# Optimization experiments

Measured on AMD Instinct MI355X. Metric: run time of the kernel, lower is better.

## Reference

```python
import jax, jax.numpy as jnp
import numpy as np

N_NODES = 50000
N_EDGES = 800000
NODE_DIM = 128
EDGE_DIM = 64
HIDDEN = 256


def setup_inputs() -> dict:
    key = jax.random.key(0)
    ks = jax.random.split(key, 12)
    glorot = lambda k, fi, fo: jax.random.normal(k, (fi, fo), jnp.float32) * (2.0 / (fi + fo)) ** 0.5
    return {
        "node_features": jax.random.normal(ks[0], (N_NODES, NODE_DIM), jnp.float32),
        "edge_features": jax.random.normal(ks[1], (N_EDGES, EDGE_DIM), jnp.float32),
        "src": jax.random.randint(ks[2], (N_EDGES,), 0, N_NODES),
        "dst": jax.random.randint(ks[3], (N_EDGES,), 0, N_NODES),
        # edge_update MLP: (2*node_dim + edge_dim) -> hidden -> edge_dim
        "We1": glorot(ks[4], 2 * NODE_DIM + EDGE_DIM, HIDDEN),
        "be1": jnp.zeros((HIDDEN,), jnp.float32),
        "We2": glorot(ks[5], HIDDEN, EDGE_DIM),
        "be2": jnp.zeros((EDGE_DIM,), jnp.float32),
        # node_update MLP: (node_dim + edge_dim) -> hidden -> node_dim
        "Wn1": glorot(ks[6], NODE_DIM + EDGE_DIM, HIDDEN),
        "bn1": jnp.zeros((HIDDEN,), jnp.float32),
        "Wn2": glorot(ks[7], HIDDEN, NODE_DIM),
        "bn2": jnp.zeros((NODE_DIM,), jnp.float32),
    }


def reference(node_features, edge_features, src, dst, We1, be1, We2, be2, Wn1, bn1, Wn2, bn2):
    # message: per-edge MLP on [src_h, e, dst_h]
    concat = jnp.concatenate(
        [node_features[src], edge_features, node_features[dst]], axis=1
    )  # [E, 2*node_dim + edge_dim]
    e_upd = jax.nn.relu(concat @ We1 + be1) @ We2 + be2  # [E, edge_dim]

    # reduce: sum incoming messages per destination node
    e_sum = jax.ops.segment_sum(e_upd, dst, num_segments=node_features.shape[0])  # [N, edge_dim]
    node_in = jnp.concatenate([node_features, e_sum], axis=1)  # [N, node_dim + edge_dim]
    h_new = jax.nn.relu(node_in @ Wn1 + bn1) @ Wn2 + bn2  # [N, node_dim]

    # DGL only applies reduce_func to nodes with at least one incoming edge
    deg = jax.ops.segment_sum(jnp.ones_like(dst, jnp.float32), dst, num_segments=node_features.shape[0])
    h_out = jnp.where(deg[:, None] > 0, h_new, node_features)

    # original module never writes e_updated back: returned edge features are the inputs
    return h_out, edge_features
```

## Files before the change

kernel.cpp:

```cpp
#include <hip/hip_runtime.h>

#define N_NODES 50000
#define N_EDGES 800000
#define NODE_DIM 128
#define EDGE_DIM 64
#define HIDDEN 256
#define K_E 320
#define K_N 192

typedef __attribute__((ext_vector_type(8))) short bf16x8;
typedef __attribute__((ext_vector_type(4))) float f32x4;
typedef unsigned short u16;
typedef unsigned int u32;

__device__ inline u16 f2bf(float f) {
  u32 u = __builtin_bit_cast(u32, f);
  u += 0x7fffu + ((u >> 16) & 1u);
  return (u16)(u >> 16);
}

__device__ inline void st_bf4(u16* p, float4 v) {
  ushort4 r;
  r.x = f2bf(v.x); r.y = f2bf(v.y); r.z = f2bf(v.z); r.w = f2bf(v.w);
  *reinterpret_cast<ushort4*>(p) = r;
}

__global__ void prep_weights(const float* __restrict__ We1, const float* __restrict__ We2,
                             const float* __restrict__ Wn1, const float* __restrict__ Wn2,
                             u16* __restrict__ we1t, u16* __restrict__ we2t,
                             u16* __restrict__ wn1t, u16* __restrict__ wn2t) {
  const int stride = gridDim.x * blockDim.x;
  const int tid = blockIdx.x * blockDim.x + threadIdx.x;
  for (int i = tid; i < HIDDEN * K_E; i += stride) {
    int n = i / K_E, k = i % K_E;
    we1t[i] = f2bf(We1[k * HIDDEN + n]);
  }
  for (int i = tid; i < EDGE_DIM * HIDDEN; i += stride) {
    int n = i / HIDDEN, k = i % HIDDEN;
    we2t[i] = f2bf(We2[k * EDGE_DIM + n]);
  }
  for (int i = tid; i < HIDDEN * K_N; i += stride) {
    int n = i / K_N, k = i % K_N;
    wn1t[i] = f2bf(Wn1[k * HIDDEN + n]);
  }
  for (int i = tid; i < NODE_DIM * HIDDEN; i += stride) {
    int n = i / HIDDEN, k = i % HIDDEN;
    wn2t[i] = f2bf(Wn2[k * NODE_DIM + n]);
  }
}

#define SA_E 328
#define SH   264

__global__ __launch_bounds__(256) void edge_kernel(
    const float* __restrict__ nf, const float* __restrict__ ef,
    const int* __restrict__ src, const int* __restrict__ dst,
    const u16* __restrict__ w1, const float* __restrict__ b1,
    const u16* __restrict__ w2, const float* __restrict__ b2,
    float* __restrict__ e_sum, float* __restrict__ degf,
    float* __restrict__ out_edge)
{
  __shared__ u16 A[64 * SA_E];
  __shared__ int sidx[64], didx[64];
  const int tid = threadIdx.x;
  const int e0 = blockIdx.x * 64;

  if (tid < 64) { sidx[tid] = src[e0 + tid]; didx[tid] = dst[e0 + tid]; }
  __syncthreads();

  const float4* nf4 = reinterpret_cast<const float4*>(nf);
  const float4* ef4 = reinterpret_cast<const float4*>(ef);
  float4* oe4 = reinterpret_cast<float4*>(out_edge);

  {
    int row = tid >> 5, c4 = tid & 31;
    #pragma unroll
    for (int p = 0; p < 8; ++p, row += 8) {
      float4 v = nf4[(size_t)sidx[row] * 32 + c4];
      st_bf4(&A[row * SA_E + c4 * 4], v);
    }
  }
  {
    #pragma unroll
    for (int p = 0; p < 4; ++p) {
      int idx = p * 256 + tid;
      int row = idx >> 4, c4 = idx & 15;
      size_t g = (size_t)(e0 + row) * 16 + c4;
      float4 v = ef4[g];
      oe4[g] = v;
      st_bf4(&A[row * SA_E + 128 + c4 * 4], v);
    }
  }
  {
    int row = tid >> 5, c4 = tid & 31;
    #pragma unroll
    for (int p = 0; p < 8; ++p, row += 8) {
      float4 v = nf4[(size_t)didx[row] * 32 + c4];
      st_bf4(&A[row * SA_E + 192 + c4 * 4], v);
    }
  }
  if (tid < 64) degf[didx[tid]] = 1.0f;
  __syncthreads();

  const int wave = tid >> 6, lane = tid & 63;
  const int lr = lane & 15;
  const int lk = (lane >> 4) * 8;

  f32x4 acc[4][4] = {};
  for (int kb = 0; kb < K_E / 32; ++kb) {
    const int ko = kb * 32 + lk;
    bf16x8 a[4], b[4];
    #pragma unroll
    for (int mt = 0; mt < 4; ++mt)
      a[mt] = *reinterpret_cast<const bf16x8*>(&A[(mt * 16 + lr) * SA_E + ko]);
    #pragma unroll
    for (int nt = 0; nt < 4; ++nt)
      b[nt] = *reinterpret_cast<const bf16x8*>(&w1[(size_t)(wave * 64 + nt * 16 + lr) * K_E + ko]);
    #pragma unroll
    for (int mt = 0; mt < 4; ++mt)
      #pragma unroll
      for (int nt = 0; nt < 4; ++nt)
        acc[mt][nt] = __builtin_amdgcn_mfma_f32_16x16x32_bf16(a[mt], b[nt], acc[mt][nt], 0, 0, 0);
  }
  __syncthreads();

  u16* H = A;
  #pragma unroll
  for (int mt = 0; mt < 4; ++mt)
    #pragma unroll
    for (int nt = 0; nt < 4; ++nt) {
      int col = wave * 64 + nt * 16 + lr;
      float bias = b1[col];
      #pragma unroll
      for (int j = 0; j < 4; ++j) {
        int row = mt * 16 + (lane >> 4) * 4 + j;
        float h = acc[mt][nt][j] + bias;
        H[row * SH + col] = f2bf(h > 0.f ? h : 0.f);
      }
    }
  __syncthreads();

  f32x4 acc2[4] = {};
  for (int kb = 0; kb < HIDDEN / 32; ++kb) {
    const int ko = kb * 32 + lk;
    bf16x8 a = *reinterpret_cast<const bf16x8*>(&H[(wave * 16 + lr) * SH + ko]);
    #pragma unroll
    for (int nt = 0; nt < 4; ++nt) {
      bf16x8 b = *reinterpret_cast<const bf16x8*>(&w2[(size_t)(nt * 16 + lr) * HIDDEN + ko]);
      acc2[nt] = __builtin_amdgcn_mfma_f32_16x16x32_bf16(a, b, acc2[nt], 0, 0, 0);
    }
  }
  #pragma unroll
  for (int nt = 0; nt < 4; ++nt) {
    int col = nt * 16 + lr;
    float bias = b2[col];
    #pragma unroll
    for (int j = 0; j < 4; ++j) {
      int row = wave * 16 + (lane >> 4) * 4 + j;
      atomicAdd(&e_sum[(size_t)didx[row] * 64 + col], acc2[nt][j] + bias);
    }
  }
}

#define SA_N 200

__global__ __launch_bounds__(256) void node_kernel(
    const float* __restrict__ nf, const float* __restrict__ e_sum,
    const float* __restrict__ degf,
    const u16* __restrict__ w1, const float* __restrict__ b1,
    const u16* __restrict__ w2, const float* __restrict__ b2,
    float* __restrict__ hout)
{
  __shared__ u16 A[64 * SH];
  const int tid = threadIdx.x;
  const int n0 = blockIdx.x * 64;

  const float4* nf4 = reinterpret_cast<const float4*>(nf);
  const float4* es4 = reinterpret_cast<const float4*>(e_sum);

  {
    int row = tid >> 5, c4 = tid & 31;
    #pragma unroll
    for (int p = 0; p < 8; ++p, row += 8) {
      int rg = min(n0 + row, N_NODES - 1);
      float4 v = nf4[(size_t)rg * 32 + c4];
      st_bf4(&A[row * SA_N + c4 * 4], v);
    }
  }
  {
    #pragma unroll
    for (int p = 0; p < 4; ++p) {
      int idx = p * 256 + tid;
      int row = idx >> 4, c4 = idx & 15;
      int rg = min(n0 + row, N_NODES - 1);
      float4 v = es4[(size_t)rg * 16 + c4];
      st_bf4(&A[row * SA_N + 128 + c4 * 4], v);
    }
  }
  __syncthreads();

  const int wave = tid >> 6, lane = tid & 63;
  const int lr = lane & 15;
  const int lk = (lane >> 4) * 8;

  f32x4 acc[4][4] = {};
  for (int kb = 0; kb < K_N / 32; ++kb) {
    const int ko = kb * 32 + lk;
    bf16x8 a[4], b[4];
    #pragma unroll
    for (int mt = 0; mt < 4; ++mt)
      a[mt] = *reinterpret_cast<const bf16x8*>(&A[(mt * 16 + lr) * SA_N + ko]);
    #pragma unroll
    for (int nt = 0; nt < 4; ++nt)
      b[nt] = *reinterpret_cast<const bf16x8*>(&w1[(size_t)(wave * 64 + nt * 16 + lr) * K_N + ko]);
    #pragma unroll
    for (int mt = 0; mt < 4; ++mt)
      #pragma unroll
      for (int nt = 0; nt < 4; ++nt)
        acc[mt][nt] = __builtin_amdgcn_mfma_f32_16x16x32_bf16(a[mt], b[nt], acc[mt][nt], 0, 0, 0);
  }
  __syncthreads();

  u16* H = A;
  #pragma unroll
  for (int mt = 0; mt < 4; ++mt)
    #pragma unroll
    for (int nt = 0; nt < 4; ++nt) {
      int col = wave * 64 + nt * 16 + lr;
      float bias = b1[col];
      #pragma unroll
      for (int j = 0; j < 4; ++j) {
        int row = mt * 16 + (lane >> 4) * 4 + j;
        float h = acc[mt][nt][j] + bias;
        H[row * SH + col] = f2bf(h > 0.f ? h : 0.f);
      }
    }
  __syncthreads();

  f32x4 acc2[8] = {};
  for (int kb = 0; kb < HIDDEN / 32; ++kb) {
    const int ko = kb * 32 + lk;
    bf16x8 a = *reinterpret_cast<const bf16x8*>(&H[(wave * 16 + lr) * SH + ko]);
    #pragma unroll
    for (int nt = 0; nt < 8; ++nt) {
      bf16x8 b = *reinterpret_cast<const bf16x8*>(&w2[(size_t)(nt * 16 + lr) * HIDDEN + ko]);
      acc2[nt] = __builtin_amdgcn_mfma_f32_16x16x32_bf16(a, b, acc2[nt], 0, 0, 0);
    }
  }
  #pragma unroll
  for (int nt = 0; nt < 8; ++nt) {
    int col = nt * 16 + lr;
    float bias = b2[col];
    #pragma unroll
    for (int j = 0; j < 4; ++j) {
      int row = wave * 16 + (lane >> 4) * 4 + j;
      int rg = n0 + row;
      if (rg < N_NODES) {
        float v = acc2[nt][j] + bias;
        hout[(size_t)rg * NODE_DIM + col] =
            (degf[rg] > 0.f) ? v : nf[(size_t)rg * NODE_DIM + col];
      }
    }
  }
}

extern "C" void kernel_launch(void* const* d_in, const int* in_sizes, int n_in,
                              void* d_out, int out_size, void* d_ws, size_t ws_size,
                              hipStream_t stream) {
  const float* nf  = (const float*)d_in[0];
  const float* ef  = (const float*)d_in[1];
  const int*   src = (const int*)d_in[2];
  const int*   dst = (const int*)d_in[3];
  const float* We1 = (const float*)d_in[4];
  const float* be1 = (const float*)d_in[5];
  const float* We2 = (const float*)d_in[6];
  const float* be2 = (const float*)d_in[7];
  const float* Wn1 = (const float*)d_in[8];
  const float* bn1 = (const float*)d_in[9];
  const float* Wn2 = (const float*)d_in[10];
  const float* bn2 = (const float*)d_in[11];

  char* ws = (char*)d_ws;
  float* e_sum = (float*)ws;
  float* degf  = (float*)(ws + 12800000);
  u16*  we1t   = (u16*)(ws + 13000000);
  u16*  we2t   = (u16*)(ws + 13163840);
  u16*  wn1t   = (u16*)(ws + 13196608);
  u16*  wn2t   = (u16*)(ws + 13294912);

  float* hout = (float*)d_out;
  float* out_edge = hout + (size_t)N_NODES * NODE_DIM;

  hipMemsetAsync(ws, 0, 13000000, stream);
  prep_weights<<<128, 256, 0, stream>>>(We1, We2, Wn1, Wn2, we1t, we2t, wn1t, wn2t);
  edge_kernel<<<N_EDGES / 64, 256, 0, stream>>>(nf, ef, src, dst, we1t, be1, we2t, be2,
                                                e_sum, degf, out_edge);
  node_kernel<<<(N_NODES + 63) / 64, 256, 0, stream>>>(nf, e_sum, degf, wn1t, bn1,
                                                       wn2t, bn2, hout);
}
```

Baseline: 631.3 us.

## Replace atomic segment-sum with counting-sort CSR gather and widen edge blocks

Builds a CSR layout of edges by destination (histogram, single-block scan, atomic rank scatter). The edge kernel then writes bf16 messages into their sorted slots, and the node kernel sums each node's messages by walking its segment, instead of issuing float atomics into e_sum. The edge kernel also moves to 512 threads with a new wave tiling (8 waves, each covering 16 rows by 128 columns). The sorted path only runs when the workspace is large enough, otherwise the atomic path is kept. It adds extra small kernels, a serial single-block scan, and bf16 rounding of each message before summation.

```diff
diff --git a/kernel.cpp b/kernel.cpp
--- a/kernel.cpp
+++ b/kernel.cpp
@@ -18,7 +18,10 @@
   u += 0x7fffu + ((u >> 16) & 1u);
   return (u16)(u >> 16);
 }
-
+__device__ inline float bf2f(u16 u) {
+  u32 x = ((u32)u) << 16;
+  return __builtin_bit_cast(float, x);
+}
 __device__ inline void st_bf4(u16* p, float4 v) {
   ushort4 r;
   r.x = f2bf(v.x); r.y = f2bf(v.y); r.z = f2bf(v.z); r.w = f2bf(v.w);
@@ -49,73 +52,252 @@
   }
 }
 
+__global__ void hist_kernel(const int* __restrict__ dst, int* __restrict__ hist) {
+  int e = blockIdx.x * blockDim.x + threadIdx.x;
+  if (e < N_EDGES) atomicAdd(&hist[dst[e]], 1);
+}
+
+#define SCAN_T 256
+#define SCAN_ITEMS 196
+__global__ void scan_kernel(const int* __restrict__ hist, int* __restrict__ off,
+                            int* __restrict__ cursor) {
+  __shared__ int ssum[SCAN_T];
+  const int tid = threadIdx.x;
+  const int base = tid * SCAN_ITEMS;
+  int s = 0;
+  for (int i = 0; i < SCAN_ITEMS; ++i) {
+    int idx = base + i;
+    s += (idx < N_NODES) ? hist[idx] : 0;
+  }
+  ssum[tid] = s;
+  __syncthreads();
+  for (int d = 1; d < SCAN_T; d <<= 1) {
+    int t = (tid >= d) ? ssum[tid - d] : 0;
+    __syncthreads();
+    ssum[tid] += t;
+    __syncthreads();
+  }
+  int run = ssum[tid] - s;
+  for (int i = 0; i < SCAN_ITEMS; ++i) {
+    int idx = base + i;
+    if (idx < N_NODES) {
+      off[idx] = run;
+      cursor[idx] = run;
+      run += hist[idx];
+    }
+  }
+  if (tid == SCAN_T - 1) off[N_NODES] = run;
+}
+
+__global__ void scatter_kernel(const int* __restrict__ dst, int* __restrict__ cursor,
+                               int* __restrict__ rank) {
+  int e = blockIdx.x * blockDim.x + threadIdx.x;
+  if (e < N_EDGES) rank[e] = atomicAdd(&cursor[dst[e]], 1);
+}
+
 #define SA_E 328
 #define SH   264
 
-__global__ __launch_bounds__(256) void edge_kernel(
+__global__ __launch_bounds__(512, 5) void edge_kernel(
     const float* __restrict__ nf, const float* __restrict__ ef,
     const int* __restrict__ src, const int* __restrict__ dst,
     const u16* __restrict__ w1, const float* __restrict__ b1,
     const u16* __restrict__ w2, const float* __restrict__ b2,
+    const int* __restrict__ rank, u16* __restrict__ e_upd,
     float* __restrict__ e_sum, float* __restrict__ degf,
-    float* __restrict__ out_edge)
+    int sorted, float* __restrict__ out_edge)
 {
   __shared__ u16 A[64 * SA_E];
-  __shared__ int sidx[64], didx[64];
+  __shared__ u16 H2[64 * 68];
+  __shared__ int sidx[64], didx[64], rk[64];
   const int tid = threadIdx.x;
   const int e0 = blockIdx.x * 64;
 
-  if (tid < 64) { sidx[tid] = src[e0 + tid]; didx[tid] = dst[e0 + tid]; }
+  if (tid < 64) {
+    sidx[tid] = src[e0 + tid];
+    didx[tid] = dst[e0 + tid];
+    rk[tid] = sorted ? rank[e0 + tid] : 0;
+  }
   __syncthreads();
 
   const float4* nf4 = reinterpret_cast<const float4*>(nf);
   const float4* ef4 = reinterpret_cast<const float4*>(ef);
   float4* oe4 = reinterpret_cast<float4*>(out_edge);
 
-  {
-    int row = tid >> 5, c4 = tid & 31;
-    #pragma unroll
-    for (int p = 0; p < 8; ++p, row += 8) {
-      float4 v = nf4[(size_t)sidx[row] * 32 + c4];
-      st_bf4(&A[row * SA_E + c4 * 4], v);
-    }
-  }
-  {
-    #pragma unroll
-    for (int p = 0; p < 4; ++p) {
-      int idx = p * 256 + tid;
-      int row = idx >> 4, c4 = idx & 15;
-      size_t g = (size_t)(e0 + row) * 16 + c4;
-      float4 v = ef4[g];
-      oe4[g] = v;
-      st_bf4(&A[row * SA_E + 128 + c4 * 4], v);
-    }
-  }
-  {
-    int row = tid >> 5, c4 = tid & 31;
-    #pragma unroll
-    for (int p = 0; p < 8; ++p, row += 8) {
-      float4 v = nf4[(size_t)didx[row] * 32 + c4];
-      st_bf4(&A[row * SA_E + 192 + c4 * 4], v);
-    }
-  }
-  if (tid < 64) degf[didx[tid]] = 1.0f;
+  #pragma unroll
+  for (int p = 0; p < 4; ++p) {
+    int i = p * 512 + tid;
+    int row = i >> 5, c4 = i & 31;
+    float4 v = nf4[(size_t)sidx[row] * 32 + c4];
+    st_bf4(&A[row * SA_E + c4 * 4], v);
+  }
+  #pragma unroll
+  for (int p = 0; p < 2; ++p) {
+    int i = p * 512 + tid;
+    int row = i >> 4, c4 = i & 15;
+    size_t g = (size_t)(e0 + row) * 16 + c4;
+    float4 v = ef4[g];
+    oe4[g] = v;
+    st_bf4(&A[row * SA_E + 128 + c4 * 4], v);
+  }
+  #pragma unroll
+  for (int p = 0; p < 4; ++p) {
+    int i = p * 512 + tid;
+    int row = i >> 5, c4 = i & 31;
+    float4 v = nf4[(size_t)didx[row] * 32 + c4];
+    st_bf4(&A[row * SA_E + 192 + c4 * 4], v);
+  }
+  if (!sorted && tid < 64) degf[didx[tid]] = 1.0f;
   __syncthreads();
 
   const int wave = tid >> 6, lane = tid & 63;
   const int lr = lane & 15;
   const int lk = (lane >> 4) * 8;
 
-  f32x4 acc[4][4] = {};
+  const int wr = wave >> 1;
+  const int wc = wave & 1;
+  f32x4 acc[8] = {};
   for (int kb = 0; kb < K_E / 32; ++kb) {
     const int ko = kb * 32 + lk;
+    bf16x8 a = *reinterpret_cast<const bf16x8*>(&A[(wr * 16 + lr) * SA_E + ko]);
+    #pragma unroll
+    for (int nt = 0; nt < 8; ++nt) {
+      bf16x8 b = *reinterpret_cast<const bf16x8*>(
+          &w1[(size_t)(wc * 128 + nt * 16 + lr) * K_E + ko]);
+      acc[nt] = __builtin_amdgcn_mfma_f32_16x16x32_bf16(a, b, acc[nt], 0, 0, 0);
+    }
+  }
+  __syncthreads();
+
+  u16* H = A;
+  #pragma unroll
+  for (int nt = 0; nt < 8; ++nt) {
+    int col = wc * 128 + nt * 16 + lr;
+    float bias = b1[col];
+    #pragma unroll
+    for (int j = 0; j < 4; ++j) {
+      int row = wr * 16 + (lane >> 4) * 4 + j;
+      float h = acc[nt][j] + bias;
+      H[row * SH + col] = f2bf(h > 0.f ? h : 0.f);
+    }
+  }
+  __syncthreads();
+
+  const int r2 = wave >> 1;
+  const int c2 = wave & 1;
+  f32x4 acc2[2] = {};
+  for (int kb = 0; kb < HIDDEN / 32; ++kb) {
+    const int ko = kb * 32 + lk;
+    bf16x8 a = *reinterpret_cast<const bf16x8*>(&H[(r2 * 16 + lr) * SH + ko]);
+    #pragma unroll
+    for (int nt = 0; nt < 2; ++nt) {
+      bf16x8 b = *reinterpret_cast<const bf16x8*>(
+          &w2[(size_t)(c2 * 32 + nt * 16 + lr) * HIDDEN + ko]);
+      acc2[nt] = __builtin_amdgcn_mfma_f32_16x16x32_bf16(a, b, acc2[nt], 0, 0, 0);
+    }
+  }
+
+  if (sorted) {
+    #pragma unroll
+    for (int nt = 0; nt < 2; ++nt) {
+      int col = c2 * 32 + nt * 16 + lr;
+      float bias = b2[col];
+      #pragma unroll
+      for (int j = 0; j < 4; ++j) {
+        int row = r2 * 16 + (lane >> 4) * 4 + j;
+        H2[row * 68 + col] = f2bf(acc2[nt][j] + bias);
+      }
+    }
+    __syncthreads();
+    #pragma unroll
+    for (int p = 0; p < 2; ++p) {
+      int i = p * 512 + tid;
+      int row = i >> 4, c = (i & 15) * 4;
+      ushort4 v = *reinterpret_cast<ushort4*>(&H2[row * 68 + c]);
+      *reinterpret_cast<ushort4*>(&e_upd[(size_t)rk[row] * 64 + c]) = v;
+    }
+  } else {
+    #pragma unroll
+    for (int nt = 0; nt < 2; ++nt) {
+      int col = c2 * 32 + nt * 16 + lr;
+      float bias = b2[col];
+      #pragma unroll
+      for (int j = 0; j < 4; ++j) {
+        int row = r2 * 16 + (lane >> 4) * 4 + j;
+        atomicAdd(&e_sum[(size_t)didx[row] * 64 + col], acc2[nt][j] + bias);
+      }
+    }
+  }
+}
+
+#define SA_N 200
+
+__global__ __launch_bounds__(256) void node_kernel(
+    const float* __restrict__ nf,
+    const u16* __restrict__ e_upd, const int* __restrict__ off,
+    const int* __restrict__ hist,
+    const float* __restrict__ e_sum, const float* __restrict__ degf,
+    const u16* __restrict__ w1, const float* __restrict__ b1,
+    const u16* __restrict__ w2, const float* __restrict__ b2,
+    int sorted, float* __restrict__ hout)
+{
+  __shared__ u16 A[64 * SH];
+  const int tid = threadIdx.x;
+  const int n0 = blockIdx.x * 64;
+
+  const float4* nf4 = reinterpret_cast<const float4*>(nf);
+
+  #pragma unroll
+  for (int p = 0; p < 8; ++p) {
+    int i = p * 256 + tid;
+    int row = i >> 5, c4 = i & 31;
+    int rg = min(n0 + row, N_NODES - 1);
+    float4 v = nf4[(size_t)rg * 32 + c4];
+    st_bf4(&A[row * SA_N + c4 * 4], v);
+  }
+
+  if (sorted) {
+    const int g = tid >> 4, l16 = tid & 15;
+    for (int row = g; row < 64; row += 16) {
+      int n = n0 + row;
+      float4 acc = {0.f, 0.f, 0.f, 0.f};
+      if (n < N_NODES) {
+        int s0 = off[n], s1 = off[n + 1];
+        for (int s = s0; s < s1; ++s) {
+          ushort4 v = *reinterpret_cast<const ushort4*>(&e_upd[(size_t)s * 64 + l16 * 4]);
+          acc.x += bf2f(v.x); acc.y += bf2f(v.y);
+          acc.z += bf2f(v.z); acc.w += bf2f(v.w);
+        }
+      }
+      st_bf4(&A[row * SA_N + 128 + l16 * 4], acc);
+    }
+  } else {
+    const float4* es4 = reinterpret_cast<const float4*>(e_sum);
+    #pragma unroll
+    for (int p = 0; p < 4; ++p) {
+      int i = p * 256 + tid;
+      int row = i >> 4, c4 = i & 15;
+      int rg = min(n0 + row, N_NODES - 1);
+      float4 v = es4[(size_t)rg * 16 + c4];
+      st_bf4(&A[row * SA_N + 128 + c4 * 4], v);
+    }
+  }
+  __syncthreads();
+
+  const int wave = tid >> 6, lane = tid & 63;
+  const int lr = lane & 15;
+  const int lk = (lane >> 4) * 8;
+
+  f32x4 acc[4][4] = {};
+  for (int kb = 0; kb < K_N / 32; ++kb) {
+    const int ko = kb * 32 + lk;
     bf16x8 a[4], b[4];
     #pragma unroll
     for (int mt = 0; mt < 4; ++mt)
-      a[mt] = *reinterpret_cast<const bf16x8*>(&A[(mt * 16 + lr) * SA_E + ko]);
+      a[mt] = *reinterpret_cast<const bf16x8*>(&A[(mt * 16 + lr) * SA_N + ko]);
     #pragma unroll
     for (int nt = 0; nt < 4; ++nt)
-      b[nt] = *reinterpret_cast<const bf16x8*>(&w1[(size_t)(wave * 64 + nt * 16 + lr) * K_E + ko]);
+      b[nt] = *reinterpret_cast<const bf16x8*>(&w1[(size_t)(wave * 64 + nt * 16 + lr) * K_N + ko]);
     #pragma unroll
     for (int mt = 0; mt < 4; ++mt)
       #pragma unroll
@@ -140,103 +322,6 @@
     }
   __syncthreads();
 
-  f32x4 acc2[4] = {};
-  for (int kb = 0; kb < HIDDEN / 32; ++kb) {
-    const int ko = kb * 32 + lk;
-    bf16x8 a = *reinterpret_cast<const bf16x8*>(&H[(wave * 16 + lr) * SH + ko]);
-    #pragma unroll
-    for (int nt = 0; nt < 4; ++nt) {
-      bf16x8 b = *reinterpret_cast<const bf16x8*>(&w2[(size_t)(nt * 16 + lr) * HIDDEN + ko]);
-      acc2[nt] = __builtin_amdgcn_mfma_f32_16x16x32_bf16(a, b, acc2[nt], 0, 0, 0);
-    }
-  }
-  #pragma unroll
-  for (int nt = 0; nt < 4; ++nt) {
-    int col = nt * 16 + lr;
-    float bias = b2[col];
-    #pragma unroll
-    for (int j = 0; j < 4; ++j) {
-      int row = wave * 16 + (lane >> 4) * 4 + j;
-      atomicAdd(&e_sum[(size_t)didx[row] * 64 + col], acc2[nt][j] + bias);
-    }
-  }
-}
-
-#define SA_N 200
-
-__global__ __launch_bounds__(256) void node_kernel(
-    const float* __restrict__ nf, const float* __restrict__ e_sum,
-    const float* __restrict__ degf,
-    const u16* __restrict__ w1, const float* __restrict__ b1,
-    const u16* __restrict__ w2, const float* __restrict__ b2,
-    float* __restrict__ hout)
-{
-  __shared__ u16 A[64 * SH];
-  const int tid = threadIdx.x;
-  const int n0 = blockIdx.x * 64;
-
-  const float4* nf4 = reinterpret_cast<const float4*>(nf);
-  const float4* es4 = reinterpret_cast<const float4*>(e_sum);
-
-  {
-    int row = tid >> 5, c4 = tid & 31;
-    #pragma unroll
-    for (int p = 0; p < 8; ++p, row += 8) {
-      int rg = min(n0 + row, N_NODES - 1);
-      float4 v = nf4[(size_t)rg * 32 + c4];
-      st_bf4(&A[row * SA_N + c4 * 4], v);
-    }
-  }
-  {
-    #pragma unroll
-    for (int p = 0; p < 4; ++p) {
-      int idx = p * 256 + tid;
-      int row = idx >> 4, c4 = idx & 15;
-      int rg = min(n0 + row, N_NODES - 1);
-      float4 v = es4[(size_t)rg * 16 + c4];
-      st_bf4(&A[row * SA_N + 128 + c4 * 4], v);
-    }
-  }
-  __syncthreads();
-
-  const int wave = tid >> 6, lane = tid & 63;
-  const int lr = lane & 15;
-  const int lk = (lane >> 4) * 8;
-
-  f32x4 acc[4][4] = {};
-  for (int kb = 0; kb < K_N / 32; ++kb) {
-    const int ko = kb * 32 + lk;
-    bf16x8 a[4], b[4];
-    #pragma unroll
-    for (int mt = 0; mt < 4; ++mt)
-      a[mt] = *reinterpret_cast<const bf16x8*>(&A[(mt * 16 + lr) * SA_N + ko]);
-    #pragma unroll
-    for (int nt = 0; nt < 4; ++nt)
-      b[nt] = *reinterpret_cast<const bf16x8*>(&w1[(size_t)(wave * 64 + nt * 16 + lr) * K_N + ko]);
-    #pragma unroll
-    for (int mt = 0; mt < 4; ++mt)
-      #pragma unroll
-      for (int nt = 0; nt < 4; ++nt)
-        acc[mt][nt] = __builtin_amdgcn_mfma_f32_16x16x32_bf16(a[mt], b[nt], acc[mt][nt], 0, 0, 0);
-  }
-  __syncthreads();
-
-  u16* H = A;
-  #pragma unroll
-  for (int mt = 0; mt < 4; ++mt)
-    #pragma unroll
-    for (int nt = 0; nt < 4; ++nt) {
-      int col = wave * 64 + nt * 16 + lr;
-      float bias = b1[col];
-      #pragma unroll
-      for (int j = 0; j < 4; ++j) {
-        int row = mt * 16 + (lane >> 4) * 4 + j;
-        float h = acc[mt][nt][j] + bias;
-        H[row * SH + col] = f2bf(h > 0.f ? h : 0.f);
-      }
-    }
-  __syncthreads();
-
   f32x4 acc2[8] = {};
   for (int kb = 0; kb < HIDDEN / 32; ++kb) {
     const int ko = kb * 32 + lk;
@@ -256,9 +341,10 @@
       int row = wave * 16 + (lane >> 4) * 4 + j;
       int rg = n0 + row;
       if (rg < N_NODES) {
+        bool has_in = sorted ? (hist[rg] != 0) : (degf[rg] > 0.f);
         float v = acc2[nt][j] + bias;
         hout[(size_t)rg * NODE_DIM + col] =
-            (degf[rg] > 0.f) ? v : nf[(size_t)rg * NODE_DIM + col];
+            has_in ? v : nf[(size_t)rg * NODE_DIM + col];
       }
     }
   }
@@ -280,21 +366,49 @@
   const float* Wn2 = (const float*)d_in[10];
   const float* bn2 = (const float*)d_in[11];
 
-  char* ws = (char*)d_ws;
-  float* e_sum = (float*)ws;
-  float* degf  = (float*)(ws + 12800000);
-  u16*  we1t   = (u16*)(ws + 13000000);
-  u16*  we2t   = (u16*)(ws + 13163840);
-  u16*  wn1t   = (u16*)(ws + 13196608);
-  u16*  wn2t   = (u16*)(ws + 13294912);
-
   float* hout = (float*)d_out;
   float* out_edge = hout + (size_t)N_NODES * NODE_DIM;
 
-  hipMemsetAsync(ws, 0, 13000000, stream);
-  prep_weights<<<128, 256, 0, stream>>>(We1, We2, Wn1, Wn2, we1t, we2t, wn1t, wn2t);
-  edge_kernel<<<N_EDGES / 64, 256, 0, stream>>>(nf, ef, src, dst, we1t, be1, we2t, be2,
-                                                e_sum, degf, out_edge);
-  node_kernel<<<(N_NODES + 63) / 64, 256, 0, stream>>>(nf, e_sum, degf, wn1t, bn1,
-                                                       wn2t, bn2, hout);
-}
+  char* ws = (char*)d_ws;
+
+  const size_t NEED_SORTED = 106560464;
+  int sorted = (ws_size >= NEED_SORTED) ? 1 : 0;
+
+  if (sorted) {
+    int* hist    = (int*)ws;
+    int* off     = (int*)(ws + 200000);
+    int* cursor  = (int*)(ws + 400016);
+    int* rank    = (int*)(ws + 600016);
+    u16* e_upd   = (u16*)(ws + 3800016);
+    u16* we1t    = (u16*)(ws + 106200016);
+    u16* we2t    = (u16*)(ws + 106363856);
+    u16* wn1t    = (u16*)(ws + 106396624);
+    u16* wn2t    = (u16*)(ws + 106494928);
+
+    hipMemsetAsync(hist, 0, 200000, stream);
+    prep_weights<<<128, 256, 0, stream>>>(We1, We2, Wn1, Wn2, we1t, we2t, wn1t, wn2t);
+    hist_kernel<<<(N_EDGES + 255) / 256, 256, 0, stream>>>(dst, hist);
+    scan_kernel<<<1, SCAN_T, 0, stream>>>(hist, off, cursor);
+    scatter_kernel<<<(N_EDGES + 255) / 256, 256, 0, stream>>>(dst, cursor, rank);
+    edge_kernel<<<N_EDGES / 64, 512, 0, stream>>>(nf, ef, src, dst, we1t, be1, we2t, be2,
+                                                  rank, e_upd, nullptr, nullptr, 1, out_edge);
+    node_kernel<<<(N_NODES + 63) / 64, 256, 0, stream>>>(nf, e_upd, off, hist,
+                                                         nullptr, nullptr,
+                                                         wn1t, bn1, wn2t, bn2, 1, hout);
+  } else {
+    float* e_sum = (float*)ws;
+    float* degf  = (float*)(ws + 12800000);
+    u16*  we1t   = (u16*)(ws + 13000000);
+    u16*  we2t   = (u16*)(ws + 13163840);
+    u16*  wn1t   = (u16*)(ws + 13196608);
+    u16*  wn2t   = (u16*)(ws + 13294912);
+
+    hipMemsetAsync(ws, 0, 13000000, stream);
+    prep_weights<<<128, 256, 0, stream>>>(We1, We2, Wn1, Wn2, we1t, we2t, wn1t, wn2t);
+    edge_kernel<<<N_EDGES / 64, 512, 0, stream>>>(nf, ef, src, dst, we1t, be1, we2t, be2,
+                                                  nullptr, nullptr, e_sum, degf, 0, out_edge);
+    node_kernel<<<(N_NODES + 63) / 64, 256, 0, stream>>>(nf, nullptr, nullptr, nullptr,
+                                                         e_sum, degf,
+                                                         wn1t, bn1, wn2t, bn2, 0, hout);
+  }
+}
```

Result: slower. 1.483 ms (+134.9%).
